# Kernel tuning notes

Measured on AMD Instinct MI355X. Metric: run time of the kernel, lower is better.

Reference implementation:

```python
import jax, jax.numpy as jnp
import numpy as np

# 5-tap image-gradient filter (cross-correlation taps, as in F.conv2d)
_K5 = (-1.0 / 12.0, 2.0 / 3.0, 0.0, -2.0 / 3.0, 1.0 / 12.0)
ALPHA = BETA = GAMMA = DELTA = 1.0
MASK_COST = 1.0
ENTROPY_WEIGHT = 1.0


def _pen(x):
    return jnp.sqrt(x + 1e-5)


def _filt_w(x):
    # depthwise 1x5 filter along W, padding 2 (matches F.conv2d(x, kernel_gx, padding=(0,2)))
    W = x.shape[-1]
    xp = jnp.pad(x, ((0, 0), (0, 0), (0, 0), (2, 2)))
    out = _K5[0] * xp[..., 0:W]
    for j in range(1, 5):
        out = out + _K5[j] * xp[..., j:j + W]
    return out


def _filt_h(x):
    # depthwise 5x1 filter along H, padding 2
    H = x.shape[-2]
    xp = jnp.pad(x, ((0, 0), (0, 0), (2, 2), (0, 0)))
    out = _K5[0] * xp[..., 0:H, :]
    for j in range(1, 5):
        out = out + _K5[j] * xp[..., j:j + H, :]
    return out


def _warp(img, flow):
    # Bilinear warp: sample img at (x + flow_x, y + flow_y); out-of-range taps contribute 0
    B, C, H, W = img.shape
    xq = jnp.arange(W, dtype=img.dtype)[None, None, :] + flow[:, 0]  # (B,H,W)
    yq = jnp.arange(H, dtype=img.dtype)[None, :, None] + flow[:, 1]
    x0 = jnp.floor(xq)
    y0 = jnp.floor(yq)
    wx1 = xq - x0
    wy1 = yq - y0
    img_flat = img.reshape(B, C, H * W)

    def tap(xi, yi, w):
        valid = (xi >= 0) & (xi <= W - 1) & (yi >= 0) & (yi <= H - 1)
        xc = jnp.clip(xi, 0, W - 1).astype(jnp.int32)
        yc = jnp.clip(yi, 0, H - 1).astype(jnp.int32)
        idx = (yc * W + xc).reshape(B, 1, H * W)
        vals = jnp.take_along_axis(img_flat, jnp.broadcast_to(idx, (B, C, H * W)), axis=2)
        vals = vals.reshape(B, C, H, W)
        return vals * (w * valid.astype(img.dtype))[:, None]

    return (tap(x0, y0, (1 - wx1) * (1 - wy1)) + tap(x0 + 1, y0, wx1 * (1 - wy1))
            + tap(x0, y0 + 1, (1 - wx1) * wy1) + tap(x0 + 1, y0 + 1, wx1 * wy1))


def _border_mask(flow):
    B, _, H, W = flow.shape
    Xp = jnp.arange(W, dtype=flow.dtype)[None, None, :] + flow[:, 0]
    Yp = jnp.arange(H, dtype=flow.dtype)[None, :, None] + flow[:, 1]
    mask_x = jax.nn.sigmoid(Xp + 0.5) * (1.0 - jax.nn.sigmoid(Xp - (W - 0.5)))
    mask_y = jax.nn.sigmoid(Yp + 0.5) * (1.0 - jax.nn.sigmoid(Yp - (H - 0.5)))
    return mask_x * mask_y


def _direction_terms(flow_a, flow_b, img_a, img_b):
    # energy terms for one direction (warping *_b by flow_a)
    mask = _border_mask(flow_a)
    flow_b_warp = _warp(flow_b, flow_a)
    mag = jnp.sum(flow_a ** 2 + flow_b_warp ** 2, axis=1)
    diff = flow_a + flow_b_warp
    occ = 1.0 - jax.nn.sigmoid(jnp.sum(diff ** 2, axis=1) - (0.01 * mag + 0.5))
    mask = mask * occ
    mask_term = MASK_COST * jnp.sum(1.0 - mask, axis=(1, 2)).mean()
    img_b_warp = _warp(img_b, flow_a)
    A = jnp.sum((img_a - img_b_warp) ** 2, axis=1)
    data_term = ALPHA * jnp.sum(_pen(A) * mask, axis=(1, 2)).mean()
    dx = flow_a[..., 1:] - flow_a[..., :-1]
    dy = flow_a[:, :, 1:, :] - flow_a[:, :, :-1, :]
    Bt = (jnp.pad(jnp.sum(dx ** 2, axis=1), ((0, 0), (0, 0), (0, 1)))
          + jnp.pad(jnp.sum(dy ** 2, axis=1), ((0, 0), (0, 1), (0, 0))))
    smooth_term = BETA * jnp.sum(_pen(Bt), axis=(1, 2)).mean()
    Ct = (jnp.sum((_filt_w(img_a) - _filt_w(img_b_warp)) ** 2, axis=1)
          + jnp.sum((_filt_h(img_a) - _filt_h(img_b_warp)) ** 2, axis=1))
    grad_term = GAMMA * jnp.sum(_pen(Ct) * mask, axis=(1, 2)).mean()
    D = jnp.sum(diff ** 2, axis=1)
    fb_part = DELTA * jnp.sum(_pen(D) * mask, axis=(1, 2)).mean()
    return mask_term + data_term + smooth_term + grad_term + fb_part


def _elbo_epe(meanf, log_varf, meanb, log_varb, img1, img2, target, noise_f, noise_b):
    # reparameterized flow samples (Nsamples = 1)
    flowf = meanf + jnp.exp(log_varf / 2.0) * noise_f
    flowb = meanb + jnp.exp(log_varb / 2.0) * noise_b
    energy = (_direction_terms(flowf, flowb, img1, img2)
              + _direction_terms(flowb, flowf, img2, img1))
    entropy = (jnp.sum(log_varf, axis=(1, 2, 3)) / 2
               + jnp.sum(log_varb, axis=(1, 2, 3)) / 2).mean()
    elbo = energy - ENTROPY_WEIGHT * entropy
    epe = jnp.sqrt(jnp.sum((meanf - target) ** 2, axis=1)).mean()
    return elbo, epe


def setup_inputs() -> dict:
    key = jax.random.key(0)
    ks = jax.random.split(key, 9)
    B, H, W = 8, 384, 512
    return {
        "meanf": jax.random.normal(ks[0], (B, 2, H, W), jnp.float32),
        "log_varf": jax.random.normal(ks[1], (B, 2, H, W), jnp.float32),
        "meanb": jax.random.normal(ks[2], (B, 2, H, W), jnp.float32),
        "log_varb": jax.random.normal(ks[3], (B, 2, H, W), jnp.float32),
        "img1": jax.random.uniform(ks[4], (B, 3, H, W), jnp.float32),
        "img2": jax.random.uniform(ks[5], (B, 3, H, W), jnp.float32),
        "target": jax.random.normal(ks[6], (B, 2, H, W), jnp.float32),
        "noise_f": jax.random.normal(ks[7], (B, 2, H, W), jnp.float32),
        "noise_b": jax.random.normal(ks[8], (B, 2, H, W), jnp.float32),
    }


def reference(meanf, log_varf, meanb, log_varb, img1, img2, target, noise_f, noise_b):
    elbo, epe = _elbo_epe(meanf, log_varf, meanb, log_varb, img1, img2, target, noise_f, noise_b)
    return (elbo, epe)
```

## Files before the change

kernel.cpp:

```cpp
#include <hip/hip_runtime.h>
#include <math.h>

#define BATCH 8
#define IH 384
#define IW 512
#define NPIX (IH*IW)
#define BN (BATCH*NPIX)

#define TW 64
#define TH 16
#define RW (TW+4)
#define RH (TH+4)
#define RN (RW*RH)
#define NTX (IW/TW)
#define NTY (IH/TH)
#define NB_DIR (NTX*NTY*BATCH*2)

#define HSX 8
#define HSY 6
#define SH (TH+2*HSY)
#define SW (TW+2*HSX)
#define SF4 (SW/4)
#define SMEM_FLOATS (3*SH*SW)
#define NITER 6

#define NB_FLOW 1536
#define ENT_OFF NB_DIR
#define EPE_OFF (ENT_OFF + NB_FLOW)
#define PART_FLOATS 8192

__device__ __forceinline__ float frcp_(float x){ return __builtin_amdgcn_rcpf(x); }
__device__ __forceinline__ float fsqrt_(float x){ return __builtin_amdgcn_sqrtf(x); }
__device__ __forceinline__ float sigmoidf_(float x){ return frcp_(1.0f + __expf(-x)); }

__device__ __forceinline__ float block_reduce_sum(float v){
    __shared__ float s[8];
    #pragma unroll
    for (int off=32; off>0; off>>=1) v += __shfl_down(v, off);
    int lane = threadIdx.x & 63, wid = threadIdx.x >> 6;
    if (lane==0) s[wid] = v;
    __syncthreads();
    float t = 0.f;
    if (wid==0){
        int nw = (blockDim.x+63)>>6;
        t = (lane < nw) ? s[lane] : 0.f;
        #pragma unroll
        for (int off=4; off>0; off>>=1) t += __shfl_down(t, off);
    }
    __syncthreads();
    return t;
}

__global__ __launch_bounds__(256)
void flows_kernel(const float* __restrict__ meanf, const float* __restrict__ log_varf,
                  const float* __restrict__ meanb, const float* __restrict__ log_varb,
                  const float* __restrict__ target,
                  const float* __restrict__ noise_f, const float* __restrict__ noise_b,
                  float* __restrict__ flowf, float* __restrict__ flowb,
                  float* __restrict__ part)
{
    int t = blockIdx.x*blockDim.x + threadIdx.x;
    const int NP4 = NPIX/4;
    int b = t / NP4, p4 = t - b*NP4;
    size_t i0 = ((size_t)b*2*NPIX)/4 + p4;
    size_t i1 = i0 + NPIX/4;

    const float4* mf = (const float4*)meanf;  const float4* lf = (const float4*)log_varf;
    const float4* mb = (const float4*)meanb;  const float4* lb = (const float4*)log_varb;
    const float4* nf = (const float4*)noise_f; const float4* nb = (const float4*)noise_b;
    const float4* tg = (const float4*)target;
    float4* ff = (float4*)flowf; float4* fbp = (float4*)flowb;

    float4 lf0 = lf[i0], lf1 = lf[i1], lb0 = lb[i0], lb1 = lb[i1];
    float4 mf0 = mf[i0], mf1 = mf[i1], mb0 = mb[i0], mb1 = mb[i1];
    float4 nf0 = nf[i0], nf1 = nf[i1], nb0 = nb[i0], nb1 = nb[i1];

    float4 o;
    o.x = mf0.x + __expf(0.5f*lf0.x)*nf0.x; o.y = mf0.y + __expf(0.5f*lf0.y)*nf0.y;
    o.z = mf0.z + __expf(0.5f*lf0.z)*nf0.z; o.w = mf0.w + __expf(0.5f*lf0.w)*nf0.w;
    ff[i0] = o;
    o.x = mf1.x + __expf(0.5f*lf1.x)*nf1.x; o.y = mf1.y + __expf(0.5f*lf1.y)*nf1.y;
    o.z = mf1.z + __expf(0.5f*lf1.z)*nf1.z; o.w = mf1.w + __expf(0.5f*lf1.w)*nf1.w;
    ff[i1] = o;
    o.x = mb0.x + __expf(0.5f*lb0.x)*nb0.x; o.y = mb0.y + __expf(0.5f*lb0.y)*nb0.y;
    o.z = mb0.z + __expf(0.5f*lb0.z)*nb0.z; o.w = mb0.w + __expf(0.5f*lb0.w)*nb0.w;
    fbp[i0] = o;
    o.x = mb1.x + __expf(0.5f*lb1.x)*nb1.x; o.y = mb1.y + __expf(0.5f*lb1.y)*nb1.y;
    o.z = mb1.z + __expf(0.5f*lb1.z)*nb1.z; o.w = mb1.w + __expf(0.5f*lb1.w)*nb1.w;
    fbp[i1] = o;

    float ent = (lf0.x+lf0.y+lf0.z+lf0.w) + (lf1.x+lf1.y+lf1.z+lf1.w)
              + (lb0.x+lb0.y+lb0.z+lb0.w) + (lb1.x+lb1.y+lb1.z+lb1.w);

    float4 t0 = tg[i0], t1 = tg[i1];
    float d0, d1, epe = 0.f;
    d0 = mf0.x - t0.x; d1 = mf1.x - t1.x; epe += fsqrt_(d0*d0 + d1*d1);
    d0 = mf0.y - t0.y; d1 = mf1.y - t1.y; epe += fsqrt_(d0*d0 + d1*d1);
    d0 = mf0.z - t0.z; d1 = mf1.z - t1.z; epe += fsqrt_(d0*d0 + d1*d1);
    d0 = mf0.w - t0.w; d1 = mf1.w - t1.w; epe += fsqrt_(d0*d0 + d1*d1);

    float s = block_reduce_sum(ent);
    if (threadIdx.x == 0) part[ENT_OFF + blockIdx.x] = s;
    float s2 = block_reduce_sum(epe);
    if (threadIdx.x == 0) part[EPE_OFF + blockIdx.x] = s2;
}

__global__ __launch_bounds__(256, 5)
void dir_kernel(const float* __restrict__ flowf, const float* __restrict__ flowb,
                const float* __restrict__ img1, const float* __restrict__ img2,
                float* __restrict__ part)
{
    __shared__ float smem[SMEM_FLOATS];
    __shared__ float mlds[TH][TW];

    const int dir = blockIdx.z & 1, b = blockIdx.z >> 1;
    const float *pfa, *pfb, *pia, *pib;
    if (dir == 0){ pfa = flowf; pfb = flowb; pia = img1; pib = img2; }
    else         { pfa = flowb; pfb = flowf; pia = img2; pib = img1; }
    pfa += (size_t)b*2*NPIX; pfb += (size_t)b*2*NPIX;
    pia += (size_t)b*3*NPIX; pib += (size_t)b*3*NPIX;

    const int tw0 = blockIdx.x*TW, th0 = blockIdx.y*TH;
    const int tid = threadIdx.x;
    float local = 0.f;

    for (int i = tid; i < 3*SH*SF4; i += 256){
        int c = i / (SH*SF4);
        int rem = i - c*(SH*SF4);
        int r = rem / SF4, c4 = rem - r*SF4;
        int gy = th0 - HSY + r;
        int gx = tw0 - HSX + 4*c4;
        float4 v = make_float4(0.f, 0.f, 0.f, 0.f);
        if (gy >= 0 && gy < IH && gx >= 0 && gx < IW){
            v = *(const float4*)(pib + (size_t)c*NPIX + gy*IW + gx);
        }
        *(float4*)&smem[c*(SH*SW) + r*SW + 4*c4] = v;
    }

    float rfax[NITER], rfay[NITER];
    #pragma unroll
    for (int it = 0; it < NITER; ++it){
        rfax[it] = 0.f; rfay[it] = 0.f;
        int i = tid + it*256;
        if (i < RN){
            int hh = i / RW, ww = i - hh*RW;
            int gh = th0 + hh - 2, gw = tw0 + ww - 2;
            if (gh >= 0 && gh < IH && gw >= 0 && gw < IW){
                int p = gh*IW + gw;
                rfax[it] = pfa[p];
                rfay[it] = pfa[NPIX + p];
            }
        }
    }
    __syncthreads();

    float rw0[NITER], rw1[NITER], rw2[NITER];
    #pragma unroll
    for (int it = 0; it < NITER; ++it){
        rw0[it] = 0.f; rw1[it] = 0.f; rw2[it] = 0.f;
        int i = tid + it*256;
        if (i >= RN) continue;
        int hh = i / RW, ww = i - hh*RW;
        int gh = th0 + hh - 2, gw = tw0 + ww - 2;
        bool inimg = (gh >= 0) && (gh < IH) && (gw >= 0) && (gw < IW);
        if (!inimg) continue;

        int p = gh*IW + gw;
        float fax = rfax[it], fay = rfay[it];
        float Xp = (float)gw + fax;
        float Yp = (float)gh + fay;

        float x0f = floorf(Xp), y0f = floorf(Yp);
        float wx1 = Xp - x0f, wy1 = Yp - y0f;
        float wx0 = 1.f - wx1, wy0 = 1.f - wy1;

        float x1f = x0f + 1.f, y1f = y0f + 1.f;
        bool vx0 = (x0f >= 0.f) && (x0f <= (float)(IW-1));
        bool vx1 = (x1f >= 0.f) && (x1f <= (float)(IW-1));
        bool vy0 = (y0f >= 0.f) && (y0f <= (float)(IH-1));
        bool vy1 = (y1f >= 0.f) && (y1f <= (float)(IH-1));
        float xc0 = fminf(fmaxf(x0f, 0.f), (float)(IW-1));
        float xc1 = fminf(fmaxf(x1f, 0.f), (float)(IW-1));
        float yc0 = fminf(fmaxf(y0f, 0.f), (float)(IH-1));
        float yc1 = fminf(fmaxf(y1f, 0.f), (float)(IH-1));
        int ix0 = (int)xc0, ix1 = (int)xc1, iy0 = (int)yc0, iy1 = (int)yc1;
        int idx0 = iy0*IW + ix0, idx1 = iy0*IW + ix1;
        int idx2 = iy1*IW + ix0, idx3 = iy1*IW + ix1;
        float wt0 = (vx0 && vy0) ? wx0*wy0 : 0.f;
        float wt1 = (vx1 && vy0) ? wx1*wy0 : 0.f;
        float wt2 = (vx0 && vy1) ? wx0*wy1 : 0.f;
        float wt3 = (vx1 && vy1) ? wx1*wy1 : 0.f;

        float w0, w1, w2;
        int lx0 = ix0 - (tw0 - HSX), ly0 = iy0 - (th0 - HSY);
        int lx1 = ix1 - (tw0 - HSX), ly1 = iy1 - (th0 - HSY);
        bool inwin = (lx0 >= 0) && (lx1 < SW) && (ly0 >= 0) && (ly1 < SH);
        if (inwin){
            int o00 = ly0*SW + lx0, o01 = ly0*SW + lx1;
            int o10 = ly1*SW + lx0, o11 = ly1*SW + lx1;
            const float* s0 = &smem[0];
            const float* s1 = s0 + SH*SW;
            const float* s2 = s1 + SH*SW;
            w0 = wt0*s0[o00] + wt1*s0[o01] + wt2*s0[o10] + wt3*s0[o11];
            w1 = wt0*s1[o00] + wt1*s1[o01] + wt2*s1[o10] + wt3*s1[o11];
            w2 = wt0*s2[o00] + wt1*s2[o01] + wt2*s2[o10] + wt3*s2[o11];
        } else {
            const float* g1 = pib + NPIX;
            const float* g2 = pib + 2*NPIX;
            w0 = wt0*pib[idx0] + wt1*pib[idx1] + wt2*pib[idx2] + wt3*pib[idx3];
            w1 = wt0*g1[idx0]  + wt1*g1[idx1]  + wt2*g1[idx2]  + wt3*g1[idx3];
            w2 = wt0*g2[idx0]  + wt1*g2[idx1]  + wt2*g2[idx2]  + wt3*g2[idx3];
        }
        rw0[it] = w0; rw1[it] = w1; rw2[it] = w2;

        bool interior = (hh >= 2) && (hh < RH-2) && (ww >= 2) && (ww < RW-2);
        if (interior){
            float mx = sigmoidf_(Xp + 0.5f) * (1.f - sigmoidf_(Xp - ((float)IW - 0.5f)));
            float my = sigmoidf_(Yp + 0.5f) * (1.f - sigmoidf_(Yp - ((float)IH - 0.5f)));
            float bm = mx * my;

            float fbwx = wt0*pfb[idx0] + wt1*pfb[idx1] + wt2*pfb[idx2] + wt3*pfb[idx3];
            const float* pfb1 = pfb + NPIX;
            float fbwy = wt0*pfb1[idx0] + wt1*pfb1[idx1] + wt2*pfb1[idx2] + wt3*pfb1[idx3];

            float mag = fax*fax + fay*fay + fbwx*fbwx + fbwy*fbwy;
            float dfx = fax + fbwx, dfy = fay + fbwy;
            float D = dfx*dfx + dfy*dfy;
            float occ = 1.f - sigmoidf_(D - (0.01f*mag + 0.5f));
            float mask = bm * occ;
            mlds[hh-2][ww-2] = mask;

            local += (1.f - mask);

            float d0 = pia[p]        - w0;
            float d1 = pia[NPIX+p]   - w1;
            float d2 = pia[2*NPIX+p] - w2;
            local += fsqrt_(d0*d0 + d1*d1 + d2*d2 + 1e-5f) * mask;

            local += fsqrt_(D + 1e-5f) * mask;

            float Bt = 0.f;
            if (gw < IW-1){
                float e0 = pfa[p+1] - fax;
                float e1 = pfa[NPIX + p+1] - fay;
                Bt += e0*e0 + e1*e1;
            }
            if (gh < IH-1){
                float e0 = pfa[p+IW] - fax;
                float e1 = pfa[NPIX + p+IW] - fay;
                Bt += e0*e0 + e1*e1;
            }
            local += fsqrt_(Bt + 1e-5f);
        }
    }
    __syncthreads();

    #pragma unroll
    for (int it = 0; it < NITER; ++it){
        int i = tid + it*256;
        if (i < RN){
            int hh = i / RW, ww = i - hh*RW;
            smem[0*(RH*RW) + hh*RW + ww] = rw0[it];
            smem[1*(RH*RW) + hh*RW + ww] = rw1[it];
            smem[2*(RH*RW) + hh*RW + ww] = rw2[it];
        }
    }
    __syncthreads();

    const float K0 = -1.f/12.f, K1 = 2.f/3.f, K3 = -2.f/3.f, K4 = 1.f/12.f;
    const float* wl0 = &smem[0];
    const float* wl1 = wl0 + RH*RW;
    const float* wl2 = wl1 + RH*RW;
    for (int i = tid; i < TW*TH; i += 256){
        int hh = i >> 6, ww = i & 63;
        int gh = th0 + hh, gw = tw0 + ww;
        int lh = hh + 2, lw = ww + 2;
        int p = gh*IW + gw;
        float Ct = 0.f;
        #pragma unroll
        for (int c = 0; c < 3; ++c){
            const float* A_ = pia + (size_t)c*NPIX;
            const float* Wl = (c == 0) ? wl0 : (c == 1) ? wl1 : wl2;
            float gxa = 0.f;
            if (gw >= 2)    gxa += K0*A_[p-2];
            if (gw >= 1)    gxa += K1*A_[p-1];
            if (gw <= IW-2) gxa += K3*A_[p+1];
            if (gw <= IW-3) gxa += K4*A_[p+2];
            float gxw = K0*Wl[lh*RW + lw-2] + K1*Wl[lh*RW + lw-1]
                      + K3*Wl[lh*RW + lw+1] + K4*Wl[lh*RW + lw+2];
            float d = gxa - gxw; Ct += d*d;
            float gya = 0.f;
            if (gh >= 2)    gya += K0*A_[p-2*IW];
            if (gh >= 1)    gya += K1*A_[p-IW];
            if (gh <= IH-2) gya += K3*A_[p+IW];
            if (gh <= IH-3) gya += K4*A_[p+2*IW];
            float gyw = K0*Wl[(lh-2)*RW + lw] + K1*Wl[(lh-1)*RW + lw]
                      + K3*Wl[(lh+1)*RW + lw] + K4*Wl[(lh+2)*RW + lw];
            d = gya - gyw; Ct += d*d;
        }
        local += fsqrt_(Ct + 1e-5f) * mlds[hh][ww];
    }

    float s = block_reduce_sum(local);
    if (tid == 0) part[blockIdx.x + NTX*(blockIdx.y + NTY*blockIdx.z)] = s;
}

__global__ __launch_bounds__(256)
void finalize_kernel(const float* __restrict__ part, float* __restrict__ out)
{
    float e = 0.f, ent = 0.f, epe = 0.f;
    for (int i = threadIdx.x; i < NB_DIR; i += 256) e += part[i];
    for (int i = threadIdx.x; i < NB_FLOW; i += 256){
        ent += part[ENT_OFF + i];
        epe += part[EPE_OFF + i];
    }
    e   = block_reduce_sum(e);
    ent = block_reduce_sum(ent);
    epe = block_reduce_sum(epe);
    if (threadIdx.x == 0){
        out[0] = e / (float)BATCH - ent / (2.f * (float)BATCH);
        out[1] = epe / ((float)BATCH * (float)NPIX);
    }
}

extern "C" void kernel_launch(void* const* d_in, const int* in_sizes, int n_in,
                              void* d_out, int out_size, void* d_ws, size_t ws_size,
                              hipStream_t stream)
{
    const float* meanf    = (const float*)d_in[0];
    const float* log_varf = (const float*)d_in[1];
    const float* meanb    = (const float*)d_in[2];
    const float* log_varb = (const float*)d_in[3];
    const float* img1     = (const float*)d_in[4];
    const float* img2     = (const float*)d_in[5];
    const float* target   = (const float*)d_in[6];
    const float* noise_f  = (const float*)d_in[7];
    const float* noise_b  = (const float*)d_in[8];

    float* ws    = (float*)d_ws;
    float* part  = ws;
    float* flowf = ws + PART_FLOATS;
    float* flowb = flowf + 2*(size_t)BN;

    const int threads = 256;

    flows_kernel<<<NB_FLOW, threads, 0, stream>>>(meanf, log_varf, meanb, log_varb,
                                                  target, noise_f, noise_b,
                                                  flowf, flowb, part);

    dim3 grid(NTX, NTY, BATCH*2);
    dir_kernel<<<grid, threads, 0, stream>>>(flowf, flowb, img1, img2, part);

    finalize_kernel<<<1, threads, 0, stream>>>(part, (float*)d_out);
}
```

Measured before the change: 267.2 us.

## Split direction kernel into warp pass and gradient pass via global buffers

```diff
diff --git a/kernel.cpp b/kernel.cpp
--- a/kernel.cpp
+++ b/kernel.cpp
@@ -11,23 +11,27 @@
 #define TH 16
 #define RW (TW+4)
 #define RH (TH+4)
-#define RN (RW*RH)
 #define NTX (IW/TW)
 #define NTY (IH/TH)
-#define NB_DIR (NTX*NTY*BATCH*2)
+#define NZ  (BATCH*2)
+#define NB_DIR (NTX*NTY*NZ)
 
 #define HSX 8
 #define HSY 6
 #define SH (TH+2*HSY)
 #define SW (TW+2*HSX)
 #define SF4 (SW/4)
-#define SMEM_FLOATS (3*SH*SW)
-#define NITER 6
+
+#define NITER_A 4
+#define NITER_OLD 6
+#define RN_OLD (RW*RH)
 
 #define NB_FLOW 1536
-#define ENT_OFF NB_DIR
+#define PA_OFF 0
+#define PB_OFF NB_DIR
+#define ENT_OFF (2*NB_DIR)
 #define EPE_OFF (ENT_OFF + NB_FLOW)
-#define PART_FLOATS 8192
+#define PART_FLOATS 16384
 
 __device__ __forceinline__ float frcp_(float x){ return __builtin_amdgcn_rcpf(x); }
 __device__ __forceinline__ float fsqrt_(float x){ return __builtin_amdgcn_sqrtf(x); }
@@ -60,6 +64,7 @@
                   float* __restrict__ part)
 {
     int t = blockIdx.x*blockDim.x + threadIdx.x;
+    if (t < NB_DIR) part[PB_OFF + t] = 0.f;
     const int NP4 = NPIX/4;
     int b = t / NP4, p4 = t - b*NP4;
     size_t i0 = ((size_t)b*2*NPIX)/4 + p4;
@@ -105,20 +110,24 @@
     if (threadIdx.x == 0) part[EPE_OFF + blockIdx.x] = s2;
 }
 
-__global__ __launch_bounds__(256, 5)
-void dir_kernel(const float* __restrict__ flowf, const float* __restrict__ flowb,
-                const float* __restrict__ img1, const float* __restrict__ img2,
-                float* __restrict__ part)
+__global__ __launch_bounds__(256, 6)
+void dirA_kernel(const float* __restrict__ flowf, const float* __restrict__ flowb,
+                 const float* __restrict__ img1, const float* __restrict__ img2,
+                 float* __restrict__ wimg, float* __restrict__ maskbuf,
+                 float* __restrict__ part)
 {
-    __shared__ float smem[SMEM_FLOATS];
-    __shared__ float mlds[TH][TW];
-
-    const int dir = blockIdx.z & 1, b = blockIdx.z >> 1;
+    __shared__ float sib[3][SH][SW];
+
+    const int z = blockIdx.z;
+    const int dir = z & 1, b = z >> 1;
     const float *pfa, *pfb, *pia, *pib;
     if (dir == 0){ pfa = flowf; pfb = flowb; pia = img1; pib = img2; }
     else         { pfa = flowb; pfb = flowf; pia = img2; pib = img1; }
     pfa += (size_t)b*2*NPIX; pfb += (size_t)b*2*NPIX;
     pia += (size_t)b*3*NPIX; pib += (size_t)b*3*NPIX;
+
+    float* wout = wimg + (size_t)z*3*NPIX;
+    float* mout = maskbuf + (size_t)z*NPIX;
 
     const int tw0 = blockIdx.x*TW, th0 = blockIdx.y*TH;
     const int tid = threadIdx.x;
@@ -134,15 +143,220 @@
         if (gy >= 0 && gy < IH && gx >= 0 && gx < IW){
             v = *(const float4*)(pib + (size_t)c*NPIX + gy*IW + gx);
         }
+        *(float4*)&sib[c][r][4*c4] = v;
+    }
+
+    float rfax[NITER_A], rfay[NITER_A];
+    #pragma unroll
+    for (int it = 0; it < NITER_A; ++it){
+        int i = tid + it*256;
+        int hh = i >> 6, ww = i & 63;
+        int p = (th0 + hh)*IW + (tw0 + ww);
+        rfax[it] = pfa[p];
+        rfay[it] = pfa[NPIX + p];
+    }
+    __syncthreads();
+
+    #pragma unroll
+    for (int it = 0; it < NITER_A; ++it){
+        int i = tid + it*256;
+        int hh = i >> 6, ww = i & 63;
+        int gh = th0 + hh, gw = tw0 + ww;
+        int p = gh*IW + gw;
+        float fax = rfax[it], fay = rfay[it];
+        float Xp = (float)gw + fax;
+        float Yp = (float)gh + fay;
+
+        float x0f = floorf(Xp), y0f = floorf(Yp);
+        float wx1 = Xp - x0f, wy1 = Yp - y0f;
+        float wx0 = 1.f - wx1, wy0 = 1.f - wy1;
+
+        float x1f = x0f + 1.f, y1f = y0f + 1.f;
+        bool vx0 = (x0f >= 0.f) && (x0f <= (float)(IW-1));
+        bool vx1 = (x1f >= 0.f) && (x1f <= (float)(IW-1));
+        bool vy0 = (y0f >= 0.f) && (y0f <= (float)(IH-1));
+        bool vy1 = (y1f >= 0.f) && (y1f <= (float)(IH-1));
+        float xc0 = fminf(fmaxf(x0f, 0.f), (float)(IW-1));
+        float xc1 = fminf(fmaxf(x1f, 0.f), (float)(IW-1));
+        float yc0 = fminf(fmaxf(y0f, 0.f), (float)(IH-1));
+        float yc1 = fminf(fmaxf(y1f, 0.f), (float)(IH-1));
+        int ix0 = (int)xc0, ix1 = (int)xc1, iy0 = (int)yc0, iy1 = (int)yc1;
+        int idx0 = iy0*IW + ix0, idx1 = iy0*IW + ix1;
+        int idx2 = iy1*IW + ix0, idx3 = iy1*IW + ix1;
+        float wt0 = (vx0 && vy0) ? wx0*wy0 : 0.f;
+        float wt1 = (vx1 && vy0) ? wx1*wy0 : 0.f;
+        float wt2 = (vx0 && vy1) ? wx0*wy1 : 0.f;
+        float wt3 = (vx1 && vy1) ? wx1*wy1 : 0.f;
+
+        float w0, w1, w2;
+        int lx0 = ix0 - (tw0 - HSX), ly0 = iy0 - (th0 - HSY);
+        int lx1 = ix1 - (tw0 - HSX), ly1 = iy1 - (th0 - HSY);
+        bool inwin = (lx0 >= 0) && (lx1 < SW) && (ly0 >= 0) && (ly1 < SH);
+        if (inwin){
+            int o00 = ly0*SW + lx0, o01 = ly0*SW + lx1;
+            int o10 = ly1*SW + lx0, o11 = ly1*SW + lx1;
+            const float* s0 = &sib[0][0][0];
+            const float* s1 = s0 + SH*SW;
+            const float* s2 = s1 + SH*SW;
+            w0 = wt0*s0[o00] + wt1*s0[o01] + wt2*s0[o10] + wt3*s0[o11];
+            w1 = wt0*s1[o00] + wt1*s1[o01] + wt2*s1[o10] + wt3*s1[o11];
+            w2 = wt0*s2[o00] + wt1*s2[o01] + wt2*s2[o10] + wt3*s2[o11];
+        } else {
+            const float* g1 = pib + NPIX;
+            const float* g2 = pib + 2*NPIX;
+            w0 = wt0*pib[idx0] + wt1*pib[idx1] + wt2*pib[idx2] + wt3*pib[idx3];
+            w1 = wt0*g1[idx0]  + wt1*g1[idx1]  + wt2*g1[idx2]  + wt3*g1[idx3];
+            w2 = wt0*g2[idx0]  + wt1*g2[idx1]  + wt2*g2[idx2]  + wt3*g2[idx3];
+        }
+
+        float mx = sigmoidf_(Xp + 0.5f) * (1.f - sigmoidf_(Xp - ((float)IW - 0.5f)));
+        float my = sigmoidf_(Yp + 0.5f) * (1.f - sigmoidf_(Yp - ((float)IH - 0.5f)));
+        float bm = mx * my;
+
+        float fbwx = wt0*pfb[idx0] + wt1*pfb[idx1] + wt2*pfb[idx2] + wt3*pfb[idx3];
+        const float* pfb1 = pfb + NPIX;
+        float fbwy = wt0*pfb1[idx0] + wt1*pfb1[idx1] + wt2*pfb1[idx2] + wt3*pfb1[idx3];
+
+        float mag = fax*fax + fay*fay + fbwx*fbwx + fbwy*fbwy;
+        float dfx = fax + fbwx, dfy = fay + fbwy;
+        float D = dfx*dfx + dfy*dfy;
+        float occ = 1.f - sigmoidf_(D - (0.01f*mag + 0.5f));
+        float mask = bm * occ;
+
+        local += (1.f - mask);
+
+        float d0 = pia[p]        - w0;
+        float d1 = pia[NPIX+p]   - w1;
+        float d2 = pia[2*NPIX+p] - w2;
+        local += fsqrt_(d0*d0 + d1*d1 + d2*d2 + 1e-5f) * mask;
+
+        local += fsqrt_(D + 1e-5f) * mask;
+
+        float Bt = 0.f;
+        if (gw < IW-1){
+            float e0 = pfa[p+1] - fax;
+            float e1 = pfa[NPIX + p+1] - fay;
+            Bt += e0*e0 + e1*e1;
+        }
+        if (gh < IH-1){
+            float e0 = pfa[p+IW] - fax;
+            float e1 = pfa[NPIX + p+IW] - fay;
+            Bt += e0*e0 + e1*e1;
+        }
+        local += fsqrt_(Bt + 1e-5f);
+
+        wout[p]          = w0;
+        wout[NPIX + p]   = w1;
+        wout[2*NPIX + p] = w2;
+        mout[p]          = mask;
+    }
+
+    float s = block_reduce_sum(local);
+    if (tid == 0) part[PA_OFF + blockIdx.x + NTX*(blockIdx.y + NTY*blockIdx.z)] = s;
+}
+
+__global__ __launch_bounds__(256, 5)
+void dirB_kernel(const float* __restrict__ img1, const float* __restrict__ img2,
+                 const float* __restrict__ wimg, const float* __restrict__ maskbuf,
+                 float* __restrict__ part)
+{
+    __shared__ float wt[3][RH][RW];
+    __shared__ float at[3][RH][RW];
+
+    const int z = blockIdx.z;
+    const int dir = z & 1, b = z >> 1;
+    const float* pia = ((dir == 0) ? img1 : img2) + (size_t)b*3*NPIX;
+    const float* wsrc = wimg + (size_t)z*3*NPIX;
+    const float* msrc = maskbuf + (size_t)z*NPIX;
+
+    const int tw0 = blockIdx.x*TW, th0 = blockIdx.y*TH;
+    const int tid = threadIdx.x;
+    float local = 0.f;
+
+    for (int i = tid; i < 3*RH*RW; i += 256){
+        int c = i / (RH*RW);
+        int rem = i - c*(RH*RW);
+        int r = rem / RW, cc = rem - r*RW;
+        int gy = th0 + r - 2;
+        int gx = tw0 + cc - 2;
+        float va = 0.f, vw = 0.f;
+        if (gy >= 0 && gy < IH && gx >= 0 && gx < IW){
+            size_t q = (size_t)c*NPIX + gy*IW + gx;
+            va = pia[q];
+            vw = wsrc[q];
+        }
+        at[c][r][cc] = va;
+        wt[c][r][cc] = vw;
+    }
+    __syncthreads();
+
+    const float K0 = -1.f/12.f, K1 = 2.f/3.f, K3 = -2.f/3.f, K4 = 1.f/12.f;
+    #pragma unroll
+    for (int it = 0; it < NITER_A; ++it){
+        int i = tid + it*256;
+        int hh = i >> 6, ww = i & 63;
+        int p = (th0 + hh)*IW + (tw0 + ww);
+        int lh = hh + 2, lw = ww + 2;
+        float Ct = 0.f;
+        #pragma unroll
+        for (int c = 0; c < 3; ++c){
+            float gxa = K0*at[c][lh][lw-2] + K1*at[c][lh][lw-1]
+                      + K3*at[c][lh][lw+1] + K4*at[c][lh][lw+2];
+            float gxw = K0*wt[c][lh][lw-2] + K1*wt[c][lh][lw-1]
+                      + K3*wt[c][lh][lw+1] + K4*wt[c][lh][lw+2];
+            float d = gxa - gxw; Ct += d*d;
+            float gya = K0*at[c][lh-2][lw] + K1*at[c][lh-1][lw]
+                      + K3*at[c][lh+1][lw] + K4*at[c][lh+2][lw];
+            float gyw = K0*wt[c][lh-2][lw] + K1*wt[c][lh-1][lw]
+                      + K3*wt[c][lh+1][lw] + K4*wt[c][lh+2][lw];
+            d = gya - gyw; Ct += d*d;
+        }
+        local += fsqrt_(Ct + 1e-5f) * msrc[p];
+    }
+
+    float s = block_reduce_sum(local);
+    if (tid == 0) part[PB_OFF + blockIdx.x + NTX*(blockIdx.y + NTY*blockIdx.z)] = s;
+}
+
+#define SMEM_FLOATS (3*SH*SW)
+__global__ __launch_bounds__(256, 5)
+void dir_kernel(const float* __restrict__ flowf, const float* __restrict__ flowb,
+                const float* __restrict__ img1, const float* __restrict__ img2,
+                float* __restrict__ part)
+{
+    __shared__ float smem[SMEM_FLOATS];
+    __shared__ float mlds[TH][TW];
+
+    const int dir = blockIdx.z & 1, b = blockIdx.z >> 1;
+    const float *pfa, *pfb, *pia, *pib;
+    if (dir == 0){ pfa = flowf; pfb = flowb; pia = img1; pib = img2; }
+    else         { pfa = flowb; pfb = flowf; pia = img2; pib = img1; }
+    pfa += (size_t)b*2*NPIX; pfb += (size_t)b*2*NPIX;
+    pia += (size_t)b*3*NPIX; pib += (size_t)b*3*NPIX;
+
+    const int tw0 = blockIdx.x*TW, th0 = blockIdx.y*TH;
+    const int tid = threadIdx.x;
+    float local = 0.f;
+
+    for (int i = tid; i < 3*SH*SF4; i += 256){
+        int c = i / (SH*SF4);
+        int rem = i - c*(SH*SF4);
+        int r = rem / SF4, c4 = rem - r*SF4;
+        int gy = th0 - HSY + r;
+        int gx = tw0 - HSX + 4*c4;
+        float4 v = make_float4(0.f, 0.f, 0.f, 0.f);
+        if (gy >= 0 && gy < IH && gx >= 0 && gx < IW){
+            v = *(const float4*)(pib + (size_t)c*NPIX + gy*IW + gx);
+        }
         *(float4*)&smem[c*(SH*SW) + r*SW + 4*c4] = v;
     }
 
-    float rfax[NITER], rfay[NITER];
-    #pragma unroll
-    for (int it = 0; it < NITER; ++it){
+    float rfax[NITER_OLD], rfay[NITER_OLD];
+    #pragma unroll
+    for (int it = 0; it < NITER_OLD; ++it){
         rfax[it] = 0.f; rfay[it] = 0.f;
         int i = tid + it*256;
-        if (i < RN){
+        if (i < RN_OLD){
             int hh = i / RW, ww = i - hh*RW;
             int gh = th0 + hh - 2, gw = tw0 + ww - 2;
             if (gh >= 0 && gh < IH && gw >= 0 && gw < IW){
@@ -154,12 +368,12 @@
     }
     __syncthreads();
 
-    float rw0[NITER], rw1[NITER], rw2[NITER];
-    #pragma unroll
-    for (int it = 0; it < NITER; ++it){
+    float rw0[NITER_OLD], rw1[NITER_OLD], rw2[NITER_OLD];
+    #pragma unroll
+    for (int it = 0; it < NITER_OLD; ++it){
         rw0[it] = 0.f; rw1[it] = 0.f; rw2[it] = 0.f;
         int i = tid + it*256;
-        if (i >= RN) continue;
+        if (i >= RN_OLD) continue;
         int hh = i / RW, ww = i - hh*RW;
         int gh = th0 + hh - 2, gw = tw0 + ww - 2;
         bool inimg = (gh >= 0) && (gh < IH) && (gw >= 0) && (gw < IW);
@@ -256,9 +470,9 @@
     __syncthreads();
 
     #pragma unroll
-    for (int it = 0; it < NITER; ++it){
+    for (int it = 0; it < NITER_OLD; ++it){
         int i = tid + it*256;
-        if (i < RN){
+        if (i < RN_OLD){
             int hh = i / RW, ww = i - hh*RW;
             smem[0*(RH*RW) + hh*RW + ww] = rw0[it];
             smem[1*(RH*RW) + hh*RW + ww] = rw1[it];
@@ -302,14 +516,14 @@
     }
 
     float s = block_reduce_sum(local);
-    if (tid == 0) part[blockIdx.x + NTX*(blockIdx.y + NTY*blockIdx.z)] = s;
+    if (tid == 0) part[PA_OFF + blockIdx.x + NTX*(blockIdx.y + NTY*blockIdx.z)] = s;
 }
 
 __global__ __launch_bounds__(256)
 void finalize_kernel(const float* __restrict__ part, float* __restrict__ out)
 {
     float e = 0.f, ent = 0.f, epe = 0.f;
-    for (int i = threadIdx.x; i < NB_DIR; i += 256) e += part[i];
+    for (int i = threadIdx.x; i < 2*NB_DIR; i += 256) e += part[i];
     for (int i = threadIdx.x; i < NB_FLOW; i += 256){
         ent += part[ENT_OFF + i];
         epe += part[EPE_OFF + i];
@@ -341,6 +555,12 @@
     float* part  = ws;
     float* flowf = ws + PART_FLOATS;
     float* flowb = flowf + 2*(size_t)BN;
+    float* wimg  = flowb + 2*(size_t)BN;
+    float* maskb = wimg + (size_t)NZ*3*NPIX;
+
+    const size_t need_bytes =
+        ((size_t)PART_FLOATS + 4*(size_t)BN + (size_t)NZ*3*NPIX + (size_t)NZ*NPIX)
+        * sizeof(float);
 
     const int threads = 256;
 
@@ -348,8 +568,14 @@
                                                   target, noise_f, noise_b,
                                                   flowf, flowb, part);
 
-    dim3 grid(NTX, NTY, BATCH*2);
-    dir_kernel<<<grid, threads, 0, stream>>>(flowf, flowb, img1, img2, part);
+    dim3 grid(NTX, NTY, NZ);
+    if (ws_size >= need_bytes){
+        dirA_kernel<<<grid, threads, 0, stream>>>(flowf, flowb, img1, img2,
+                                                  wimg, maskb, part);
+        dirB_kernel<<<grid, threads, 0, stream>>>(img1, img2, wimg, maskb, part);
+    } else {
+        dir_kernel<<<grid, threads, 0, stream>>>(flowf, flowb, img1, img2, part);
+    }
 
     finalize_kernel<<<1, threads, 0, stream>>>(part, (float*)d_out);
 }
```

Measured after the change: 241.4 us. 9.7% less time.
